# Kernel optimization log

Hardware: AMD Instinct MI355X
Metric: run time of the kernel (lower is better)

Reference implementation:

```python
import jax, jax.numpy as jnp
import numpy as np

H = 256
B, S = 8, 2048
WIN = 16


def setup_inputs() -> dict:
    key = jax.random.key(0)
    k1, k2, k3, k4, k5 = jax.random.split(key, 5)
    bound = 1.0 / np.sqrt(H)  # torch nn.RNN init range
    x = jax.random.normal(k1, (B, S, H), dtype=jnp.float32)
    W_ih = jax.random.uniform(k2, (H, H), jnp.float32, -bound, bound)
    W_hh = jax.random.uniform(k3, (H, H), jnp.float32, -bound, bound)
    b_ih = jax.random.uniform(k4, (H,), jnp.float32, -bound, bound)
    b_hh = jax.random.uniform(k5, (H,), jnp.float32, -bound, bound)
    return {"x": x, "W_ih": W_ih, "W_hh": W_hh, "b_ih": b_ih, "b_hh": b_hh, "window": WIN}


def reference(x, W_ih, W_hh, b_ih, b_hh, window):
    # Original: get_K builds [B, S, window, H] overlapping windows (left-padded
    # with window-1 zeros), runs an RNN over each length-`window` sequence with
    # h0 = 0, and keeps the last hidden state -> [B, S, H].
    # Equivalent streaming form: at step k of the window, every position t
    # consumes xpad[:, t + k]; so slice a shifted view of the padded input and
    # update all B*S hidden states at once (never materializing the windows).
    b, s, h = x.shape
    xpad = jnp.pad(x, ((0, 0), (window - 1, 0), (0, 0)))  # [B, S+W-1, H]

    def step(hid, k):
        xk = jax.lax.dynamic_slice(xpad, (0, k, 0), (b, s, h))  # [B, S, H]
        hid = jnp.tanh(xk @ W_ih.T + b_ih + hid @ W_hh.T + b_hh)
        return hid, None

    h0 = jnp.zeros((b, s, h), dtype=x.dtype)
    h_last, _ = jax.lax.scan(step, h0, jnp.arange(window))
    return h_last  # [B, S, H]
```

## Files before the change

kernel.cpp:

```cpp
#include <hip/hip_runtime.h>

#define HDIM 256
#define SEQ 2048
#define TPOS 32

typedef _Float16 half8_t __attribute__((ext_vector_type(8)));
typedef float floatx16 __attribute__((ext_vector_type(16)));

#define U_PITCH 1024
#define H_PITCH 512
#define U_ROWS 47
#define H0_OFF (U_ROWS * U_PITCH)
#define H1_OFF (H0_OFF + 32 * H_PITCH)
#define LDS_BYTES (H0_OFF + 2 * 32 * H_PITCH)

static __device__ __forceinline__ float exp2f_fast(float x) {
  float r; asm("v_exp_f32 %0, %1" : "=v"(r) : "v"(x)); return r;
}
static __device__ __forceinline__ float rcpf_fast(float x) {
  float r; asm("v_rcp_f32 %0, %1" : "=v"(r) : "v"(x)); return r;
}
static __device__ __forceinline__ float tanhf_fast(float x) {
  float e = exp2f_fast(x * 2.8853900817779268f);
  return 1.0f - 2.0f * rcpf_fast(e + 1.0f);
}
static __device__ __forceinline__ unsigned pkh(float a, float b) {
  return __builtin_bit_cast(unsigned, __builtin_amdgcn_cvt_pkrtz(a, b));
}

__global__ __launch_bounds__(256, 2) void winrnn_kernel(
    const float* __restrict__ x, const float* __restrict__ W_ih,
    const float* __restrict__ W_hh, const float* __restrict__ b_ih,
    const float* __restrict__ b_hh, float* __restrict__ out) {
  extern __shared__ char smem[];
  const int tid = threadIdx.x;
  const int w = tid >> 6;
  const int lane = tid & 63;
  const int l31 = lane & 31;
  const int hi = lane >> 5;

  const int wg = blockIdx.x;
  const int batch = wg >> 6;
  const int t0 = (wg & 63) * TPOS;
  const float* xb = x + (size_t)batch * SEQ * HDIM;

  const int jbase = w * 64;
  const int p_loc = l31;
  const int hswz = l31 << 4;

  {
    char* xl = smem + H0_OFF;
#pragma unroll
    for (int it = 0; it < 16; ++it) {
      int idx = tid + it * 256;
      int row = idx >> 6;
      int c4 = idx & 63;
      int xi = t0 - 15 + row;
      float4 v = make_float4(0.f, 0.f, 0.f, 0.f);
      if (row < U_ROWS && xi >= 0)
        v = *reinterpret_cast<const float4*>(xb + (size_t)xi * HDIM + c4 * 4);
      uint2 u;
      u.x = pkh(v.x, v.y);
      u.y = pkh(v.z, v.w);
      *reinterpret_cast<uint2*>(xl + row * H_PITCH + ((c4 * 8) ^ ((row & 31) << 4))) = u;
    }
  }

  half8_t Wf[2][16];
#pragma unroll
  for (int jt = 0; jt < 2; ++jt)
#pragma unroll
    for (int kt = 0; kt < 16; ++kt) {
      const float* wp = W_ih + (size_t)(jbase + jt * 32 + l31) * HDIM + kt * 16 + hi * 8;
      float4 a = *reinterpret_cast<const float4*>(wp);
      float4 b = *reinterpret_cast<const float4*>(wp + 4);
      uint4 uu;
      uu.x = pkh(a.x, a.y); uu.y = pkh(a.z, a.w);
      uu.z = pkh(b.x, b.y); uu.w = pkh(b.z, b.w);
      Wf[jt][kt] = __builtin_bit_cast(half8_t, uu);
    }

  float4 biasf[2][4];
#pragma unroll
  for (int jt = 0; jt < 2; ++jt)
#pragma unroll
    for (int g = 0; g < 4; ++g) {
      int j0 = jbase + jt * 32 + g * 8 + hi * 4;
      float4 bi = *reinterpret_cast<const float4*>(b_ih + j0);
      float4 bh = *reinterpret_cast<const float4*>(b_hh + j0);
      biasf[jt][g] = make_float4(bi.x + bh.x, bi.y + bh.y, bi.z + bh.z, bi.w + bh.w);
    }

  __syncthreads();

  {
    const char* xl = smem + H0_OFF;
    char* Ul = smem;
#pragma unroll
    for (int s = 0; s < 2; ++s) {
      int prow = s * 32 + l31;
      floatx16 acc0, acc1;
#pragma unroll
      for (int g = 0; g < 4; ++g) {
        acc0[4*g+0] = biasf[0][g].x; acc0[4*g+1] = biasf[0][g].y;
        acc0[4*g+2] = biasf[0][g].z; acc0[4*g+3] = biasf[0][g].w;
        acc1[4*g+0] = biasf[1][g].x; acc1[4*g+1] = biasf[1][g].y;
        acc1[4*g+2] = biasf[1][g].z; acc1[4*g+3] = biasf[1][g].w;
      }
#pragma unroll
      for (int kt = 0; kt < 16; ++kt) {
        half8_t xB = *reinterpret_cast<const half8_t*>(
            xl + prow * H_PITCH + ((kt * 32 + hi * 16) ^ ((prow & 31) << 4)));
        acc0 = __builtin_amdgcn_mfma_f32_32x32x16_f16(Wf[0][kt], xB, acc0, 0, 0, 0);
        acc1 = __builtin_amdgcn_mfma_f32_32x32x16_f16(Wf[1][kt], xB, acc1, 0, 0, 0);
      }
      if (prow < U_ROWS) {
#pragma unroll
        for (int jt = 0; jt < 2; ++jt)
#pragma unroll
          for (int g = 0; g < 4; ++g) {
            int j0 = jbase + jt * 32 + g * 8 + hi * 4;
            float4 st;
            const floatx16& ac = jt ? acc1 : acc0;
            st.x = ac[4*g+0]; st.y = ac[4*g+1]; st.z = ac[4*g+2]; st.w = ac[4*g+3];
            *reinterpret_cast<float4*>(Ul + prow * U_PITCH + ((j0 * 4) ^ ((prow & 31) << 4))) = st;
          }
      }
    }
  }

#pragma unroll
  for (int jt = 0; jt < 2; ++jt)
#pragma unroll
    for (int kt = 0; kt < 16; ++kt) {
      const float* wp = W_hh + (size_t)(jbase + jt * 32 + l31) * HDIM + kt * 16 + hi * 8;
      float4 a = *reinterpret_cast<const float4*>(wp);
      float4 b = *reinterpret_cast<const float4*>(wp + 4);
      uint4 uu;
      uu.x = pkh(a.x, a.y); uu.y = pkh(a.z, a.w);
      uu.z = pkh(b.x, b.y); uu.w = pkh(b.z, b.w);
      Wf[jt][kt] = __builtin_bit_cast(half8_t, uu);
    }

  __syncthreads();

  const char* Ul = smem;
  char* hb0 = smem + H0_OFF;
  char* hb1 = smem + H1_OFF;

  floatx16 acc0, acc1;
  for (int k = 0; k < 16; ++k) {
    int urow = p_loc + k;
    int uswz = (urow & 31) << 4;
#pragma unroll
    for (int g = 0; g < 4; ++g) {
      int j00 = (jbase + g * 8 + hi * 4) * 4;
      float4 u0 = *reinterpret_cast<const float4*>(Ul + urow * U_PITCH + (j00 ^ uswz));
      float4 u1 = *reinterpret_cast<const float4*>(Ul + urow * U_PITCH + ((j00 + 128) ^ uswz));
      acc0[4*g+0] = u0.x; acc0[4*g+1] = u0.y; acc0[4*g+2] = u0.z; acc0[4*g+3] = u0.w;
      acc1[4*g+0] = u1.x; acc1[4*g+1] = u1.y; acc1[4*g+2] = u1.z; acc1[4*g+3] = u1.w;
    }
    if (k > 0) {
      const char* hr = ((k & 1) ? hb0 : hb1);
#pragma unroll
      for (int kt = 0; kt < 16; ++kt) {
        half8_t hB = *reinterpret_cast<const half8_t*>(
            hr + p_loc * H_PITCH + ((kt * 32 + hi * 16) ^ hswz));
        acc0 = __builtin_amdgcn_mfma_f32_32x32x16_f16(Wf[0][kt], hB, acc0, 0, 0, 0);
        acc1 = __builtin_amdgcn_mfma_f32_32x32x16_f16(Wf[1][kt], hB, acc1, 0, 0, 0);
      }
    }
    if (k < 15) {
      char* hw = ((k & 1) ? hb1 : hb0);
#pragma unroll
      for (int jt = 0; jt < 2; ++jt) {
        const floatx16& ac = jt ? acc1 : acc0;
#pragma unroll
        for (int g = 0; g < 4; ++g) {
          float ta = tanhf_fast(ac[4*g+0]);
          float tb = tanhf_fast(ac[4*g+1]);
          float tc = tanhf_fast(ac[4*g+2]);
          float td = tanhf_fast(ac[4*g+3]);
          uint2 u; u.x = pkh(ta, tb); u.y = pkh(tc, td);
          int jb = (jbase + jt * 32 + g * 8 + hi * 4) * 2;
          *reinterpret_cast<uint2*>(hw + p_loc * H_PITCH + (jb ^ hswz)) = u;
        }
      }
      __syncthreads();
    }
  }

  __syncthreads();
  {
    char* ol = smem + H0_OFF;
    const int oswz = (p_loc & 31) << 4;
#pragma unroll
    for (int jt = 0; jt < 2; ++jt) {
      const floatx16& ac = jt ? acc1 : acc0;
#pragma unroll
      for (int g = 0; g < 4; ++g) {
        float4 st;
        st.x = tanhf_fast(ac[4*g+0]); st.y = tanhf_fast(ac[4*g+1]);
        st.z = tanhf_fast(ac[4*g+2]); st.w = tanhf_fast(ac[4*g+3]);
        int jb = (jbase + jt * 32 + g * 8 + hi * 4) * 4;
        *reinterpret_cast<float4*>(ol + p_loc * 1024 + (jb ^ oswz)) = st;
      }
    }
  }
  __syncthreads();
  {
    const char* ol = smem + H0_OFF;
    float* ob = out + ((size_t)batch * SEQ + t0) * HDIM;
#pragma unroll
    for (int it = 0; it < 8; ++it) {
      int idx = tid + it * 256;
      int row = idx >> 6;
      int c = idx & 63;
      float4 v = *reinterpret_cast<const float4*>(
          ol + row * 1024 + ((c * 16) ^ ((row & 31) << 4)));
      *reinterpret_cast<float4*>(ob + (size_t)row * HDIM + c * 4) = v;
    }
  }
}

extern "C" void kernel_launch(void* const* d_in, const int* in_sizes, int n_in,
                              void* d_out, int out_size, void* d_ws, size_t ws_size,
                              hipStream_t stream) {
  const float* x    = (const float*)d_in[0];
  const float* W_ih = (const float*)d_in[1];
  const float* W_hh = (const float*)d_in[2];
  const float* b_ih = (const float*)d_in[3];
  const float* b_hh = (const float*)d_in[4];
  float* out = (float*)d_out;
  static_assert(2 * LDS_BYTES <= 160 * 1024, "need 2 WGs/CU");
  hipFuncSetAttribute(reinterpret_cast<const void*>(winrnn_kernel),
                      hipFuncAttributeMaxDynamicSharedMemorySize, LDS_BYTES);
  winrnn_kernel<<<dim3(512), dim3(256), LDS_BYTES, stream>>>(x, W_ih, W_hh, b_ih, b_hh, out);
}
```

Measured before the change: 73.37 us.

## Split hidden dim across eight waves and use rational tanh approximation

Doubles the workgroup to 512 threads so each wave owns 32 output columns instead of 64, halving per-wave MFMA chains, weight registers and accumulators. The aim is more waves available to hide latency during the 16-step serial recurrence. It also replaces the exp/rcp tanh with a clamped Padé rational polynomial plus one reciprocal. The trade-offs are more waves contending at each per-step barrier and a slightly different tanh accuracy.

```diff
diff --git a/kernel.cpp b/kernel.cpp
--- a/kernel.cpp
+++ b/kernel.cpp
@@ -14,21 +14,21 @@
 #define H1_OFF (H0_OFF + 32 * H_PITCH)
 #define LDS_BYTES (H0_OFF + 2 * 32 * H_PITCH)
 
-static __device__ __forceinline__ float exp2f_fast(float x) {
-  float r; asm("v_exp_f32 %0, %1" : "=v"(r) : "v"(x)); return r;
-}
 static __device__ __forceinline__ float rcpf_fast(float x) {
   float r; asm("v_rcp_f32 %0, %1" : "=v"(r) : "v"(x)); return r;
 }
 static __device__ __forceinline__ float tanhf_fast(float x) {
-  float e = exp2f_fast(x * 2.8853900817779268f);
-  return 1.0f - 2.0f * rcpf_fast(e + 1.0f);
+  x = fminf(fmaxf(x, -4.97f), 4.97f);
+  float t = x * x;
+  float N = ((t + 378.f) * t + 17325.f) * t + 135135.f;
+  float D = ((28.f * t + 3150.f) * t + 62370.f) * t + 135135.f;
+  return (x * N) * rcpf_fast(D);
 }
 static __device__ __forceinline__ unsigned pkh(float a, float b) {
   return __builtin_bit_cast(unsigned, __builtin_amdgcn_cvt_pkrtz(a, b));
 }
 
-__global__ __launch_bounds__(256, 2) void winrnn_kernel(
+__global__ __launch_bounds__(512, 4) void winrnn_kernel(
     const float* __restrict__ x, const float* __restrict__ W_ih,
     const float* __restrict__ W_hh, const float* __restrict__ b_ih,
     const float* __restrict__ b_hh, float* __restrict__ out) {
@@ -44,15 +44,15 @@
   const int t0 = (wg & 63) * TPOS;
   const float* xb = x + (size_t)batch * SEQ * HDIM;
 
-  const int jbase = w * 64;
+  const int jbase = w * 32;
   const int p_loc = l31;
   const int hswz = l31 << 4;
 
   {
     char* xl = smem + H0_OFF;
 #pragma unroll
-    for (int it = 0; it < 16; ++it) {
-      int idx = tid + it * 256;
+    for (int it = 0; it < 8; ++it) {
+      int idx = tid + it * 512;
       int row = idx >> 6;
       int c4 = idx & 63;
       int xi = t0 - 15 + row;
@@ -66,30 +66,26 @@
     }
   }
 
-  half8_t Wf[2][16];
-#pragma unroll
-  for (int jt = 0; jt < 2; ++jt)
-#pragma unroll
-    for (int kt = 0; kt < 16; ++kt) {
-      const float* wp = W_ih + (size_t)(jbase + jt * 32 + l31) * HDIM + kt * 16 + hi * 8;
-      float4 a = *reinterpret_cast<const float4*>(wp);
-      float4 b = *reinterpret_cast<const float4*>(wp + 4);
-      uint4 uu;
-      uu.x = pkh(a.x, a.y); uu.y = pkh(a.z, a.w);
-      uu.z = pkh(b.x, b.y); uu.w = pkh(b.z, b.w);
-      Wf[jt][kt] = __builtin_bit_cast(half8_t, uu);
-    }
-
-  float4 biasf[2][4];
-#pragma unroll
-  for (int jt = 0; jt < 2; ++jt)
-#pragma unroll
-    for (int g = 0; g < 4; ++g) {
-      int j0 = jbase + jt * 32 + g * 8 + hi * 4;
-      float4 bi = *reinterpret_cast<const float4*>(b_ih + j0);
-      float4 bh = *reinterpret_cast<const float4*>(b_hh + j0);
-      biasf[jt][g] = make_float4(bi.x + bh.x, bi.y + bh.y, bi.z + bh.z, bi.w + bh.w);
-    }
+  half8_t Wf[16];
+#pragma unroll
+  for (int kt = 0; kt < 16; ++kt) {
+    const float* wp = W_ih + (size_t)(jbase + l31) * HDIM + kt * 16 + hi * 8;
+    float4 a = *reinterpret_cast<const float4*>(wp);
+    float4 b = *reinterpret_cast<const float4*>(wp + 4);
+    uint4 uu;
+    uu.x = pkh(a.x, a.y); uu.y = pkh(a.z, a.w);
+    uu.z = pkh(b.x, b.y); uu.w = pkh(b.z, b.w);
+    Wf[kt] = __builtin_bit_cast(half8_t, uu);
+  }
+
+  float4 biasf[4];
+#pragma unroll
+  for (int g = 0; g < 4; ++g) {
+    int j0 = jbase + g * 8 + hi * 4;
+    float4 bi = *reinterpret_cast<const float4*>(b_ih + j0);
+    float4 bh = *reinterpret_cast<const float4*>(b_hh + j0);
+    biasf[g] = make_float4(bi.x + bh.x, bi.y + bh.y, bi.z + bh.z, bi.w + bh.w);
+  }
 
   __syncthreads();
 
@@ -99,48 +95,40 @@
 #pragma unroll
     for (int s = 0; s < 2; ++s) {
       int prow = s * 32 + l31;
-      floatx16 acc0, acc1;
+      floatx16 acc;
 #pragma unroll
       for (int g = 0; g < 4; ++g) {
-        acc0[4*g+0] = biasf[0][g].x; acc0[4*g+1] = biasf[0][g].y;
-        acc0[4*g+2] = biasf[0][g].z; acc0[4*g+3] = biasf[0][g].w;
-        acc1[4*g+0] = biasf[1][g].x; acc1[4*g+1] = biasf[1][g].y;
-        acc1[4*g+2] = biasf[1][g].z; acc1[4*g+3] = biasf[1][g].w;
+        acc[4*g+0] = biasf[g].x; acc[4*g+1] = biasf[g].y;
+        acc[4*g+2] = biasf[g].z; acc[4*g+3] = biasf[g].w;
       }
 #pragma unroll
       for (int kt = 0; kt < 16; ++kt) {
         half8_t xB = *reinterpret_cast<const half8_t*>(
             xl + prow * H_PITCH + ((kt * 32 + hi * 16) ^ ((prow & 31) << 4)));
-        acc0 = __builtin_amdgcn_mfma_f32_32x32x16_f16(Wf[0][kt], xB, acc0, 0, 0, 0);
-        acc1 = __builtin_amdgcn_mfma_f32_32x32x16_f16(Wf[1][kt], xB, acc1, 0, 0, 0);
+        acc = __builtin_amdgcn_mfma_f32_32x32x16_f16(Wf[kt], xB, acc, 0, 0, 0);
       }
       if (prow < U_ROWS) {
 #pragma unroll
-        for (int jt = 0; jt < 2; ++jt)
-#pragma unroll
-          for (int g = 0; g < 4; ++g) {
-            int j0 = jbase + jt * 32 + g * 8 + hi * 4;
-            float4 st;
-            const floatx16& ac = jt ? acc1 : acc0;
-            st.x = ac[4*g+0]; st.y = ac[4*g+1]; st.z = ac[4*g+2]; st.w = ac[4*g+3];
-            *reinterpret_cast<float4*>(Ul + prow * U_PITCH + ((j0 * 4) ^ ((prow & 31) << 4))) = st;
-          }
-      }
-    }
-  }
-
-#pragma unroll
-  for (int jt = 0; jt < 2; ++jt)
-#pragma unroll
-    for (int kt = 0; kt < 16; ++kt) {
-      const float* wp = W_hh + (size_t)(jbase + jt * 32 + l31) * HDIM + kt * 16 + hi * 8;
-      float4 a = *reinterpret_cast<const float4*>(wp);
-      float4 b = *reinterpret_cast<const float4*>(wp + 4);
-      uint4 uu;
-      uu.x = pkh(a.x, a.y); uu.y = pkh(a.z, a.w);
-      uu.z = pkh(b.x, b.y); uu.w = pkh(b.z, b.w);
-      Wf[jt][kt] = __builtin_bit_cast(half8_t, uu);
-    }
+        for (int g = 0; g < 4; ++g) {
+          int j0 = jbase + g * 8 + hi * 4;
+          float4 st;
+          st.x = acc[4*g+0]; st.y = acc[4*g+1]; st.z = acc[4*g+2]; st.w = acc[4*g+3];
+          *reinterpret_cast<float4*>(Ul + prow * U_PITCH + ((j0 * 4) ^ ((prow & 31) << 4))) = st;
+        }
+      }
+    }
+  }
+
+#pragma unroll
+  for (int kt = 0; kt < 16; ++kt) {
+    const float* wp = W_hh + (size_t)(jbase + l31) * HDIM + kt * 16 + hi * 8;
+    float4 a = *reinterpret_cast<const float4*>(wp);
+    float4 b = *reinterpret_cast<const float4*>(wp + 4);
+    uint4 uu;
+    uu.x = pkh(a.x, a.y); uu.y = pkh(a.z, a.w);
+    uu.z = pkh(b.x, b.y); uu.w = pkh(b.z, b.w);
+    Wf[kt] = __builtin_bit_cast(half8_t, uu);
+  }
 
   __syncthreads();
 
@@ -148,7 +136,7 @@
   char* hb0 = smem + H0_OFF;
   char* hb1 = smem + H1_OFF;
 
-  floatx16 acc0, acc1;
+  floatx16 acc;
   for (int k = 0; k < 16; ++k) {
     int urow = p_loc + k;
     int uswz = (urow & 31) << 4;
@@ -156,9 +144,7 @@
     for (int g = 0; g < 4; ++g) {
       int j00 = (jbase + g * 8 + hi * 4) * 4;
       float4 u0 = *reinterpret_cast<const float4*>(Ul + urow * U_PITCH + (j00 ^ uswz));
-      float4 u1 = *reinterpret_cast<const float4*>(Ul + urow * U_PITCH + ((j00 + 128) ^ uswz));
-      acc0[4*g+0] = u0.x; acc0[4*g+1] = u0.y; acc0[4*g+2] = u0.z; acc0[4*g+3] = u0.w;
-      acc1[4*g+0] = u1.x; acc1[4*g+1] = u1.y; acc1[4*g+2] = u1.z; acc1[4*g+3] = u1.w;
+      acc[4*g+0] = u0.x; acc[4*g+1] = u0.y; acc[4*g+2] = u0.z; acc[4*g+3] = u0.w;
     }
     if (k > 0) {
       const char* hr = ((k & 1) ? hb0 : hb1);
@@ -166,25 +152,20 @@
       for (int kt = 0; kt < 16; ++kt) {
         half8_t hB = *reinterpret_cast<const half8_t*>(
             hr + p_loc * H_PITCH + ((kt * 32 + hi * 16) ^ hswz));
-        acc0 = __builtin_amdgcn_mfma_f32_32x32x16_f16(Wf[0][kt], hB, acc0, 0, 0, 0);
-        acc1 = __builtin_amdgcn_mfma_f32_32x32x16_f16(Wf[1][kt], hB, acc1, 0, 0, 0);
+        acc = __builtin_amdgcn_mfma_f32_32x32x16_f16(Wf[kt], hB, acc, 0, 0, 0);
       }
     }
     if (k < 15) {
       char* hw = ((k & 1) ? hb1 : hb0);
 #pragma unroll
-      for (int jt = 0; jt < 2; ++jt) {
-        const floatx16& ac = jt ? acc1 : acc0;
-#pragma unroll
-        for (int g = 0; g < 4; ++g) {
-          float ta = tanhf_fast(ac[4*g+0]);
-          float tb = tanhf_fast(ac[4*g+1]);
-          float tc = tanhf_fast(ac[4*g+2]);
-          float td = tanhf_fast(ac[4*g+3]);
-          uint2 u; u.x = pkh(ta, tb); u.y = pkh(tc, td);
-          int jb = (jbase + jt * 32 + g * 8 + hi * 4) * 2;
-          *reinterpret_cast<uint2*>(hw + p_loc * H_PITCH + (jb ^ hswz)) = u;
-        }
+      for (int g = 0; g < 4; ++g) {
+        float ta = tanhf_fast(acc[4*g+0]);
+        float tb = tanhf_fast(acc[4*g+1]);
+        float tc = tanhf_fast(acc[4*g+2]);
+        float td = tanhf_fast(acc[4*g+3]);
+        uint2 u; u.x = pkh(ta, tb); u.y = pkh(tc, td);
+        int jb = (jbase + g * 8 + hi * 4) * 2;
+        *reinterpret_cast<uint2*>(hw + p_loc * H_PITCH + (jb ^ hswz)) = u;
       }
       __syncthreads();
     }
@@ -193,18 +174,14 @@
   __syncthreads();
   {
     char* ol = smem + H0_OFF;
-    const int oswz = (p_loc & 31) << 4;
-#pragma unroll
-    for (int jt = 0; jt < 2; ++jt) {
-      const floatx16& ac = jt ? acc1 : acc0;
-#pragma unroll
-      for (int g = 0; g < 4; ++g) {
-        float4 st;
-        st.x = tanhf_fast(ac[4*g+0]); st.y = tanhf_fast(ac[4*g+1]);
-        st.z = tanhf_fast(ac[4*g+2]); st.w = tanhf_fast(ac[4*g+3]);
-        int jb = (jbase + jt * 32 + g * 8 + hi * 4) * 4;
-        *reinterpret_cast<float4*>(ol + p_loc * 1024 + (jb ^ oswz)) = st;
-      }
+    const int oswz = p_loc << 4;
+#pragma unroll
+    for (int g = 0; g < 4; ++g) {
+      float4 st;
+      st.x = tanhf_fast(acc[4*g+0]); st.y = tanhf_fast(acc[4*g+1]);
+      st.z = tanhf_fast(acc[4*g+2]); st.w = tanhf_fast(acc[4*g+3]);
+      int jb4 = (jbase + g * 8 + hi * 4) * 4;
+      *reinterpret_cast<float4*>(ol + p_loc * 1024 + (jb4 ^ oswz)) = st;
     }
   }
   __syncthreads();
@@ -212,8 +189,8 @@
     const char* ol = smem + H0_OFF;
     float* ob = out + ((size_t)batch * SEQ + t0) * HDIM;
 #pragma unroll
-    for (int it = 0; it < 8; ++it) {
-      int idx = tid + it * 256;
+    for (int it = 0; it < 4; ++it) {
+      int idx = tid + it * 512;
       int row = idx >> 6;
       int c = idx & 63;
       float4 v = *reinterpret_cast<const float4*>(
@@ -235,5 +212,5 @@
   static_assert(2 * LDS_BYTES <= 160 * 1024, "need 2 WGs/CU");
   hipFuncSetAttribute(reinterpret_cast<const void*>(winrnn_kernel),
                       hipFuncAttributeMaxDynamicSharedMemorySize, LDS_BYTES);
-  winrnn_kernel<<<dim3(512), dim3(256), LDS_BYTES, stream>>>(x, W_ih, W_hh, b_ih, b_hh, out);
-}
+  winrnn_kernel<<<dim3(512), dim3(512), LDS_BYTES, stream>>>(x, W_ih, W_hh, b_ih, b_hh, out);
+}
```

Result: slower. 87.99 us (+19.9%).
